# Performance work log

Measured on AMD Instinct MI355X. Metric: run time of the kernel, lower is better.

Reference implementation:

```python
import jax, jax.numpy as jnp
import numpy as np

BS, J, L, D = 32, 4, 512, 768  # batch, entity sentences, max_bert_len, bert_embed_dim
K = 4                          # num_entity_per_sentence; J*K == num_candidates == 16
OUT = 256                      # entity_final_output_dim


def setup_inputs() -> dict:
    key = jax.random.key(0)
    k1, k2, k3, k4 = jax.random.split(key, 4)
    zipped_entity = jax.random.normal(k1, (BS, J, L, D), dtype=jnp.float32)
    # strictly increasing separator indices per (b, j); spans are [last+1, sep)
    steps = jax.random.randint(k2, (BS, J, K), 5, 60)
    entity_token_sep_idx = 1 + jnp.cumsum(steps, axis=-1)  # values < 1+4*60 < L
    W = jax.random.normal(k3, (D, OUT), dtype=jnp.float32) * 0.02
    b = jax.random.normal(k4, (OUT,), dtype=jnp.float32) * 0.02
    return {"zipped_entity": zipped_entity,
            "entity_token_sep_idx": entity_token_sep_idx,
            "W": W, "b": b}


def reference(zipped_entity, entity_token_sep_idx, W, b):
    # Ragged per-entity span mean-pool, vectorized via a span mask, then Linear.
    sep = entity_token_sep_idx                                    # [bs, J, K]
    starts = jnp.concatenate([jnp.ones_like(sep[..., :1]), sep[..., :-1] + 1], axis=-1)
    ends = sep                                                    # exclusive
    t = jnp.arange(L)                                             # token positions
    # mask[b,j,k,l] = 1 if token l belongs to entity k of sentence j
    mask = ((t[None, None, None, :] >= starts[..., None]) &
            (t[None, None, None, :] < ends[..., None])).astype(zipped_entity.dtype)
    sums = jnp.einsum('bjkl,bjld->bjkd', mask, zipped_entity)     # [bs, J, K, D]
    counts = (ends - starts).astype(zipped_entity.dtype)[..., None]
    pooled = sums / counts                                        # mean over span
    bs = zipped_entity.shape[0]
    # entity_idx = k + j*K -> reshape [bs, J, K, D] to [bs, num_candidates, D]
    encoded_entity = pooled.reshape(bs, J * K, D)
    return encoded_entity @ W + b                                 # final Linear
```

## Files before the change

### kernel.cpp

```cpp
#include <hip/hip_runtime.h>
#include <hip/hip_bf16.h>

#define BS  32
#define J   4
#define L   512
#define D   768
#define K   4
#define OUT 256

typedef float f4 __attribute__((ext_vector_type(4)));

#define PROW 3456

__global__ __launch_bounds__(256) void pool_kernel(
    const float* __restrict__ Z,
    const int*   __restrict__ sep,
    float*       __restrict__ ws)
{
    __shared__ float part[4][PROW];

    const int blk  = blockIdx.x;
    const int e    = blk >> 1, h = blk & 1;
    const int sent = e >> 2,  k = e & 3;
    const int end   = sep[sent * K + k];
    const int prev  = (k == 0) ? 0 : sep[sent * K + k - 1];
    const int start = prev + 1;
    const float inv = 1.0f / (float)(end - start);

    const int w    = threadIdx.x >> 6;
    const int lane = threadIdx.x & 63;
    const float* zbase = Z + (size_t)sent * L * D + lane * 4;

    f4 a0={0,0,0,0}, a1={0,0,0,0}, a2={0,0,0,0};
    f4 c0={0,0,0,0}, c1={0,0,0,0}, c2={0,0,0,0};

    int l = start + h + 2 * w;
    for (; l + 8 < end; l += 16) {
        const float* r0 = zbase + (size_t)l * D;
        const float* r1 = zbase + (size_t)(l + 8) * D;
        a0 += *(const f4*)(r0);       a1 += *(const f4*)(r0 + 256);
        a2 += *(const f4*)(r0 + 512);
        c0 += *(const f4*)(r1);       c1 += *(const f4*)(r1 + 256);
        c2 += *(const f4*)(r1 + 512);
    }
    if (l < end) {
        const float* r0 = zbase + (size_t)l * D;
        a0 += *(const f4*)(r0);       a1 += *(const f4*)(r0 + 256);
        a2 += *(const f4*)(r0 + 512);
    }
    a0 += c0; a1 += c1; a2 += c2;

    *(f4*)&part[w][lane*4]       = a0;
    *(f4*)&part[w][lane*4 + 256] = a1;
    *(f4*)&part[w][lane*4 + 512] = a2;
    __syncthreads();

    const int t = threadIdx.x;
    if (t < 192) {
        f4 s = {0,0,0,0};
        #pragma unroll
        for (int ww = 0; ww < 4; ++ww) s += *(const f4*)&part[ww][t*4];
        s *= inv;
        *(f4*)&ws[(((size_t)sent*2 + h)*K + k) * D + t*4] = s;
    }
}

__global__ __launch_bounds__(256) void gemm_kernel(
    const float* __restrict__ ws,
    const float* __restrict__ W,
    const float* __restrict__ bias,
    float*       __restrict__ out)
{
    const int g  = blockIdx.x >> 2;
    const int cq = blockIdx.x & 3;

    __shared__ float p[K * D];
    __shared__ float red[16][K][64];
    {
        const f4* a = (const f4*)(ws + (size_t)g * 2 * K * D);
        #pragma unroll
        for (int i = threadIdx.x; i < (K * D) / 4; i += 256) {
            f4 v = a[i] + a[i + (K * D) / 4];
            *(f4*)&p[i * 4] = v;
        }
    }
    __syncthreads();

    const int w    = threadIdx.x >> 6;
    const int lane = threadIdx.x & 63;
    const int dg   = lane >> 4;
    const int cl   = lane & 15;
    const int colbase = cq * 64 + cl * 4;
    const int dbase   = w * 192 + dg;

    f4 acc0={0,0,0,0}, acc1={0,0,0,0}, acc2={0,0,0,0}, acc3={0,0,0,0};
    #pragma unroll 4
    for (int i = 0; i < 48; ++i) {
        const int d = dbase + 4 * i;
        f4 wv = *(const f4*)&W[(size_t)d * OUT + colbase];
        acc0 += p[0 * D + d] * wv;
        acc1 += p[1 * D + d] * wv;
        acc2 += p[2 * D + d] * wv;
        acc3 += p[3 * D + d] * wv;
    }

    const int r = w * 4 + dg;
    *(f4*)&red[r][0][cl * 4] = acc0;
    *(f4*)&red[r][1][cl * 4] = acc1;
    *(f4*)&red[r][2][cl * 4] = acc2;
    *(f4*)&red[r][3][cl * 4] = acc3;
    __syncthreads();

    const int e2  = threadIdx.x >> 6;
    const int col = threadIdx.x & 63;
    float s = bias[cq * 64 + col];
    #pragma unroll
    for (int rr = 0; rr < 16; ++rr) s += red[rr][e2][col];
    out[(size_t)(g * K + e2) * OUT + cq * 64 + col] = s;
}

extern "C" void kernel_launch(void* const* d_in, const int* in_sizes, int n_in,
                              void* d_out, int out_size, void* d_ws, size_t ws_size,
                              hipStream_t stream) {
    const float* Z    = (const float*)d_in[0];
    const int*   sep  = (const int*)d_in[1];
    const float* W    = (const float*)d_in[2];
    const float* bias = (const float*)d_in[3];
    float*       out  = (float*)d_out;
    float*       ws   = (float*)d_ws;

    pool_kernel<<<2 * BS * J * K, 256, 0, stream>>>(Z, sep, ws);
    gemm_kernel<<<BS * J * K, 256, 0, stream>>>(ws, W, bias, out);
}
```

Before: 23.18 us.

## Fuse pooling and GEMM into one launch with per-sentence atomic counters

Merges the pooling and linear kernels into a single grid. The first 1024 blocks pool spans and signal a per-sentence counter, and the remaining 512 blocks spin-wait on that counter before doing the GEMM slice. The goal is to remove the second kernel launch and the inter-kernel gap, and to let GEMM for early sentences overlap with pooling of later ones. In exchange it adds a memset launch for the counters, spin-waiting that relies on the producer blocks being scheduled before the consumers, and shared memory held in a union.

```diff
diff --git a/kernel.cpp b/kernel.cpp
--- a/kernel.cpp
+++ b/kernel.cpp
@@ -10,84 +10,97 @@
 
 typedef float f4 __attribute__((ext_vector_type(4)));
 
-#define PROW 3456
-
-__global__ __launch_bounds__(256) void pool_kernel(
+__global__ __launch_bounds__(256) void fused_kernel(
     const float* __restrict__ Z,
     const int*   __restrict__ sep,
-    float*       __restrict__ ws)
+    const float* __restrict__ W,
+    const float* __restrict__ bias,
+    float*       __restrict__ out,
+    float*       __restrict__ ws,
+    int*         __restrict__ cnt)
 {
-    __shared__ float part[4][PROW];
+    __shared__ union {
+        float part[4][D];
+        struct {
+            float p[K * D];
+            float red[16][K][64];
+        } bb;
+    } sm;
 
-    const int blk  = blockIdx.x;
-    const int e    = blk >> 1, h = blk & 1;
-    const int sent = e >> 2,  k = e & 3;
-    const int end   = sep[sent * K + k];
-    const int prev  = (k == 0) ? 0 : sep[sent * K + k - 1];
-    const int start = prev + 1;
-    const float inv = 1.0f / (float)(end - start);
+    const int blk = blockIdx.x;
+    const int tid = threadIdx.x;
 
-    const int w    = threadIdx.x >> 6;
-    const int lane = threadIdx.x & 63;
-    const float* zbase = Z + (size_t)sent * L * D + lane * 4;
+    if (blk < 1024) {
+        const int e    = blk >> 1, h = blk & 1;
+        const int sent = e >> 2,  k = e & 3;
+        const int end   = sep[sent * K + k];
+        const int prev  = (k == 0) ? 0 : sep[sent * K + k - 1];
+        const int start = prev + 1;
+        const float inv = 1.0f / (float)(end - start);
 
-    f4 a0={0,0,0,0}, a1={0,0,0,0}, a2={0,0,0,0};
-    f4 c0={0,0,0,0}, c1={0,0,0,0}, c2={0,0,0,0};
+        const int w    = tid >> 6;
+        const int lane = tid & 63;
+        const float* zbase = Z + (size_t)sent * L * D + lane * 4;
 
-    int l = start + h + 2 * w;
-    for (; l + 8 < end; l += 16) {
-        const float* r0 = zbase + (size_t)l * D;
-        const float* r1 = zbase + (size_t)(l + 8) * D;
-        a0 += *(const f4*)(r0);       a1 += *(const f4*)(r0 + 256);
-        a2 += *(const f4*)(r0 + 512);
-        c0 += *(const f4*)(r1);       c1 += *(const f4*)(r1 + 256);
-        c2 += *(const f4*)(r1 + 512);
+        f4 a0={0,0,0,0}, a1={0,0,0,0}, a2={0,0,0,0};
+        f4 c0={0,0,0,0}, c1={0,0,0,0}, c2={0,0,0,0};
+
+        int l = start + h + 2 * w;
+        for (; l + 8 < end; l += 16) {
+            const float* r0 = zbase + (size_t)l * D;
+            const float* r1 = zbase + (size_t)(l + 8) * D;
+            a0 += *(const f4*)(r0);       a1 += *(const f4*)(r0 + 256);
+            a2 += *(const f4*)(r0 + 512);
+            c0 += *(const f4*)(r1);       c1 += *(const f4*)(r1 + 256);
+            c2 += *(const f4*)(r1 + 512);
+        }
+        if (l < end) {
+            const float* r0 = zbase + (size_t)l * D;
+            a0 += *(const f4*)(r0);       a1 += *(const f4*)(r0 + 256);
+            a2 += *(const f4*)(r0 + 512);
+        }
+        a0 += c0; a1 += c1; a2 += c2;
+
+        *(f4*)&sm.part[w][lane*4]       = a0;
+        *(f4*)&sm.part[w][lane*4 + 256] = a1;
+        *(f4*)&sm.part[w][lane*4 + 512] = a2;
+        __syncthreads();
+
+        if (tid < 192) {
+            f4 s = {0,0,0,0};
+            #pragma unroll
+            for (int ww = 0; ww < 4; ++ww) s += *(const f4*)&sm.part[ww][tid*4];
+            s *= inv;
+            *(f4*)&ws[(((size_t)sent*2 + h)*K + k) * D + tid*4] = s;
+        }
+        __syncthreads();
+        if (tid == 0)
+            __hip_atomic_fetch_add(&cnt[sent], 1, __ATOMIC_RELEASE,
+                                   __HIP_MEMORY_SCOPE_AGENT);
+        return;
     }
-    if (l < end) {
-        const float* r0 = zbase + (size_t)l * D;
-        a0 += *(const f4*)(r0);       a1 += *(const f4*)(r0 + 256);
-        a2 += *(const f4*)(r0 + 512);
+
+    const int t  = blk - 1024;
+    const int g  = t >> 2;
+    const int cq = t & 3;
+
+    if (tid == 0) {
+        while (__hip_atomic_load(&cnt[g], __ATOMIC_ACQUIRE,
+                                 __HIP_MEMORY_SCOPE_AGENT) != 8)
+            __builtin_amdgcn_s_sleep(8);
     }
-    a0 += c0; a1 += c1; a2 += c2;
-
-    *(f4*)&part[w][lane*4]       = a0;
-    *(f4*)&part[w][lane*4 + 256] = a1;
-    *(f4*)&part[w][lane*4 + 512] = a2;
     __syncthreads();
 
-    const int t = threadIdx.x;
-    if (t < 192) {
-        f4 s = {0,0,0,0};
-        #pragma unroll
-        for (int ww = 0; ww < 4; ++ww) s += *(const f4*)&part[ww][t*4];
-        s *= inv;
-        *(f4*)&ws[(((size_t)sent*2 + h)*K + k) * D + t*4] = s;
-    }
-}
-
-__global__ __launch_bounds__(256) void gemm_kernel(
-    const float* __restrict__ ws,
-    const float* __restrict__ W,
-    const float* __restrict__ bias,
-    float*       __restrict__ out)
-{
-    const int g  = blockIdx.x >> 2;
-    const int cq = blockIdx.x & 3;
-
-    __shared__ float p[K * D];
-    __shared__ float red[16][K][64];
     {
         const f4* a = (const f4*)(ws + (size_t)g * 2 * K * D);
         #pragma unroll
-        for (int i = threadIdx.x; i < (K * D) / 4; i += 256) {
-            f4 v = a[i] + a[i + (K * D) / 4];
-            *(f4*)&p[i * 4] = v;
-        }
+        for (int i = tid; i < (K * D) / 4; i += 256)
+            *(f4*)&sm.bb.p[i * 4] = a[i] + a[i + (K * D) / 4];
     }
     __syncthreads();
 
-    const int w    = threadIdx.x >> 6;
-    const int lane = threadIdx.x & 63;
+    const int w    = tid >> 6;
+    const int lane = tid & 63;
     const int dg   = lane >> 4;
     const int cl   = lane & 15;
     const int colbase = cq * 64 + cl * 4;
@@ -98,24 +111,24 @@
     for (int i = 0; i < 48; ++i) {
         const int d = dbase + 4 * i;
         f4 wv = *(const f4*)&W[(size_t)d * OUT + colbase];
-        acc0 += p[0 * D + d] * wv;
-        acc1 += p[1 * D + d] * wv;
-        acc2 += p[2 * D + d] * wv;
-        acc3 += p[3 * D + d] * wv;
+        acc0 += sm.bb.p[0 * D + d] * wv;
+        acc1 += sm.bb.p[1 * D + d] * wv;
+        acc2 += sm.bb.p[2 * D + d] * wv;
+        acc3 += sm.bb.p[3 * D + d] * wv;
     }
 
     const int r = w * 4 + dg;
-    *(f4*)&red[r][0][cl * 4] = acc0;
-    *(f4*)&red[r][1][cl * 4] = acc1;
-    *(f4*)&red[r][2][cl * 4] = acc2;
-    *(f4*)&red[r][3][cl * 4] = acc3;
+    *(f4*)&sm.bb.red[r][0][cl * 4] = acc0;
+    *(f4*)&sm.bb.red[r][1][cl * 4] = acc1;
+    *(f4*)&sm.bb.red[r][2][cl * 4] = acc2;
+    *(f4*)&sm.bb.red[r][3][cl * 4] = acc3;
     __syncthreads();
 
-    const int e2  = threadIdx.x >> 6;
-    const int col = threadIdx.x & 63;
+    const int e2  = tid >> 6;
+    const int col = tid & 63;
     float s = bias[cq * 64 + col];
     #pragma unroll
-    for (int rr = 0; rr < 16; ++rr) s += red[rr][e2][col];
+    for (int rr = 0; rr < 16; ++rr) s += sm.bb.red[rr][e2][col];
     out[(size_t)(g * K + e2) * OUT + cq * 64 + col] = s;
 }
 
@@ -128,7 +141,8 @@
     const float* bias = (const float*)d_in[3];
     float*       out  = (float*)d_out;
     float*       ws   = (float*)d_ws;
+    int*         cnt  = (int*)(ws + (size_t)128 * 2 * K * D);
 
-    pool_kernel<<<2 * BS * J * K, 256, 0, stream>>>(Z, sep, ws);
-    gemm_kernel<<<BS * J * K, 256, 0, stream>>>(ws, W, bias, out);
+    hipMemsetAsync(cnt, 0, 128 * sizeof(int), stream);
+    fused_kernel<<<1536, 256, 0, stream>>>(Z, sep, W, bias, out, ws, cnt);
 }
```

After: 81.84 us. +253.1%, slower.
